# Optimization experiments

Hardware: AMD Instinct MI355X
Metric: run time of the kernel (lower is better)

Reference implementation:

```python
import jax, jax.numpy as jnp
import numpy as np

N = 8192        # n_nodes
NFEAT = 512
NHID = 256
AVG_DEG = 32
K = 64          # mean_kwargs k
TEMP = 1.0      # mean_kwargs temperature


def setup_inputs() -> dict:
    key = jax.random.key(0)
    ks = jax.random.split(key, 5)
    x = jax.random.normal(ks[0], (N, NFEAT), jnp.float32)
    edge_index = jax.random.randint(ks[1], (2, N * AVG_DEG), 0, N, dtype=jnp.int64)
    W1 = jax.random.normal(ks[2], (NFEAT, NHID), jnp.float32) / np.sqrt(NFEAT)
    b1 = jnp.zeros((NHID,), jnp.float32)
    W2 = jax.random.normal(ks[3], (NHID, NHID), jnp.float32) / np.sqrt(NHID)
    b2 = jnp.zeros((NHID,), jnp.float32)
    return {"x": x, "edge_index": edge_index, "W1": W1, "b1": b1, "W2": W2, "b2": b2}


def _gcn_norm(edge_index, n, dtype):
    # PyG gcn_norm: add self-loops (weight 1), deg over col, sym normalization
    loops = jnp.arange(n, dtype=edge_index.dtype)
    row = jnp.concatenate([edge_index[0], loops])
    col = jnp.concatenate([edge_index[1], loops])
    w = jnp.ones(row.shape[0], dtype)
    deg = jnp.zeros((n,), dtype).at[col].add(w)
    dis = jnp.where(deg > 0, jax.lax.rsqrt(jnp.where(deg > 0, deg, 1.0)), 0.0)
    return row, col, dis[row] * w * dis[col]


def _soft_k_medoid(row, col, w, x):
    # soft_weighted_medoid_k_neighborhood(A, x, k=K, temperature=TEMP, with_weight_correction=True)
    n, d = x.shape
    A = jnp.zeros((n, n), x.dtype).at[row, col].add(w)   # coalesced dense adjacency
    topk_a, topk_idx = jax.lax.top_k(A, K)               # [n, K] neighbor weights / ids
    xk = x[topk_idx]                                     # [n, K, d]
    sq = jnp.sum(xk * xk, axis=-1)                       # [n, K]
    G = jnp.einsum('nkd,nld->nkl', xk, xk)               # Gram per node
    d2 = jnp.maximum(sq[:, :, None] + sq[:, None, :] - 2.0 * G, 0.0)
    pos = d2 > 0
    dist = jnp.where(pos, jnp.sqrt(jnp.where(pos, d2, 1.0)), 0.0)  # safe sqrt (grad-safe)
    # weighted sum of distances to each top-k candidate j: c[n,j] = sum_l a[n,l] * ||x_l - x_j||
    c = jnp.einsum('nl,nlj->nj', topk_a, dist)
    c = jnp.where(topk_a == 0, jnp.finfo(x.dtype).max, c)
    soft = jax.nn.softmax(-c / TEMP, axis=-1)            # [n, K]
    soft = soft * topk_a                                 # with_weight_correction
    soft = soft / jnp.sum(soft, axis=-1, keepdims=True)
    row_sum = jnp.sum(A, axis=-1)                        # preserve neighborhood mass
    return row_sum[:, None] * jnp.einsum('nk,nkd->nd', soft, xk)


def reference(x, edge_index, W1, b1, W2, b2):
    n = x.shape[0]
    row, col, w = _gcn_norm(edge_index, n, x.dtype)
    h = jax.nn.relu(_soft_k_medoid(row, col, w, x @ W1) + b1)   # gc1 + relu (dropout: eval = identity)
    return jax.nn.relu(_soft_k_medoid(row, col, w, h @ W2) + b2)  # gc2 + relu
```

## Files before the change

kernel.cpp:

```cpp
#include <hip/hip_runtime.h>

typedef _Float16 half2v __attribute__((ext_vector_type(2)));
typedef _Float16 half4 __attribute__((ext_vector_type(4)));
typedef _Float16 half8 __attribute__((ext_vector_type(8)));
typedef float f32x4 __attribute__((ext_vector_type(4)));

#define NNODE 8192
#define NHID  256
#define RCAP  128
#define KCAP  64

__global__ void k_init(int* deg, int* rowcnt, int* flag, const void* edges) {
    int i = blockIdx.x * blockDim.x + threadIdx.x;
    if (i < NNODE) { deg[i] = 0; rowcnt[i] = 0; }
    if (i == 0) {
        const long long* e = (const long long*)edges;
        int ok = 1;
        for (int k = 0; k < 64; ++k) { long long v = e[k]; if (v < 0 || v >= NNODE) ok = 0; }
        *flag = ok;
    }
}

__global__ void k_build(const void* edges, const int* flag, int* rowcnt, int* nbr,
                        int* deg, int E) {
    int i = blockIdx.x * blockDim.x + threadIdx.x;
    int total = E + NNODE;
    if (i >= total) return;
    int r, c;
    if (i < E) {
        if (*flag) {
            const long long* e = (const long long*)edges;
            r = (int)e[i]; c = (int)e[E + i];
        } else {
            const int* e = (const int*)edges;
            r = e[i]; c = e[E + i];
        }
    } else { r = i - E; c = r; }
    int pos = atomicAdd(&rowcnt[r], 1);
    if (pos < RCAP) nbr[r * RCAP + pos] = c;
    atomicAdd(&deg[c], 1);
}

__global__ __launch_bounds__(128) void k_dedup(const int* __restrict__ nbr,
                                               const int* __restrict__ rowcnt,
                                               const int* __restrict__ deg,
                                               int* __restrict__ cols,
                                               float* __restrict__ wout,
                                               float* __restrict__ rsum) {
    __shared__ int lc[RCAP];
    __shared__ float lw[RCAP];
    __shared__ unsigned char kp[RCAP];
    __shared__ int s_cw[2];
    __shared__ float s_rw[2];
    const int r = blockIdx.x, t = threadIdx.x;
    const int wid = t >> 6, lane = t & 63;
    int n = rowcnt[r]; if (n > RCAP) n = RCAP;
    if (t < n) lc[t] = nbr[r * RCAP + t];
    __syncthreads();
    float dr = 1.f / sqrtf((float)deg[r]);
    bool keep = false; float wv = 0.f;
    if (t < n) {
        int c = lc[t];
        int mult = 0; bool first = true;
        for (int i = 0; i < n; ++i) {
            int ci = lc[i];
            if (ci == c) { mult++; if (i < t) first = false; }
        }
        keep = first;
        if (first) wv = (float)mult * dr * (1.f / sqrtf((float)deg[c]));
    }
    kp[t] = keep ? 1 : 0; lw[t] = wv;
    float rv = wv;
#pragma unroll
    for (int d = 1; d < 64; d <<= 1) rv += __shfl_xor(rv, d, 64);
    unsigned long long b = __ballot(keep);
    int pre = __popcll(b & ((1ull << lane) - 1ull));
    int cw = __popcll(b);
    if (lane == 0) { s_cw[wid] = cw; s_rw[wid] = rv; }
    __syncthreads();
    int total = s_cw[0] + s_cw[1];
    if (t == 0) rsum[r] = s_rw[0] + s_rw[1];
    const int base = r * KCAP;
    if (total <= KCAP) {
        int off = (wid ? s_cw[0] : 0) + pre;
        if (keep) { cols[base + off] = lc[t]; wout[base + off] = wv; }
        for (int m = total + t; m < KCAP; m += 128) { cols[base + m] = r; wout[base + m] = 0.f; }
    } else if (t == 0) {
        for (int s = 0; s < KCAP; ++s) {
            int best = -1;
            for (int i = 0; i < n; ++i) {
                if (!kp[i]) continue;
                if (best < 0 || lw[i] > lw[best] ||
                    (lw[i] == lw[best] && lc[i] < lc[best])) best = i;
            }
            cols[base + s] = lc[best]; wout[base + s] = lw[best]; kp[best] = 0;
        }
    }
}

__global__ void k_splitT(const float* __restrict__ W, _Float16* __restrict__ hiT, int Kdim) {
    int idx = blockIdx.x * 256 + threadIdx.x;
    if (idx >= Kdim * NHID) return;
    int k = idx >> 8, n = idx & 255;
    hiT[(size_t)n * Kdim + k] = (_Float16)W[idx];
}

#define GLS 72

__global__ __launch_bounds__(256) void k_gemm(
    const float* __restrict__ Af32, const _Float16* __restrict__ Ahi,
    const _Float16* __restrict__ BT, _Float16* __restrict__ Chi, int K, int af32) {
    __shared__ _Float16 sA[64][GLS];
    __shared__ _Float16 sB[64][GLS];
    const int t = threadIdx.x;
    const int bm = blockIdx.x * 64, bn = blockIdx.y * 64;
    const int lane = t & 63, L15 = lane & 15, q = lane >> 4;
    const int w = t >> 6, wr = w >> 1, wc = w & 1;
    f32x4 acc[2][2];
#pragma unroll
    for (int a = 0; a < 2; ++a)
#pragma unroll
        for (int b = 0; b < 2; ++b) acc[a][b] = (f32x4){0.f, 0.f, 0.f, 0.f};

    for (int k0 = 0; k0 < K; k0 += 64) {
        if (af32) {
#pragma unroll
            for (int i = 0; i < 4; ++i) {
                int row = i * 16 + (t >> 4), kc = (t & 15) * 4;
                float4 v = *(const float4*)(Af32 + (size_t)(bm + row) * K + k0 + kc);
                half4 h;
                h[0] = (_Float16)v.x; h[1] = (_Float16)v.y;
                h[2] = (_Float16)v.z; h[3] = (_Float16)v.w;
                *(half4*)&sA[row][kc] = h;
            }
        } else {
#pragma unroll
            for (int i = 0; i < 2; ++i) {
                int row = i * 32 + (t >> 3), ch = t & 7;
                *(half8*)&sA[row][ch * 8] =
                    *(const half8*)(Ahi + (size_t)(bm + row) * K + k0 + ch * 8);
            }
        }
#pragma unroll
        for (int i = 0; i < 2; ++i) {
            int row = i * 32 + (t >> 3), ch = t & 7;
            *(half8*)&sB[row][ch * 8] =
                *(const half8*)(BT + (size_t)(bn + row) * K + k0 + ch * 8);
        }
        __syncthreads();
#pragma unroll
        for (int ks = 0; ks < 2; ++ks) {
            const int ko = ks * 32 + q * 8;
            half8 ah[2], bh[2];
#pragma unroll
            for (int tr = 0; tr < 2; ++tr)
                ah[tr] = *(const half8*)&sA[32 * wr + 16 * tr + L15][ko];
#pragma unroll
            for (int tc = 0; tc < 2; ++tc)
                bh[tc] = *(const half8*)&sB[32 * wc + 16 * tc + L15][ko];
#pragma unroll
            for (int tr = 0; tr < 2; ++tr)
#pragma unroll
                for (int tc = 0; tc < 2; ++tc)
                    acc[tr][tc] = __builtin_amdgcn_mfma_f32_16x16x32_f16(ah[tr], bh[tc], acc[tr][tc], 0, 0, 0);
        }
        __syncthreads();
    }
#pragma unroll
    for (int tr = 0; tr < 2; ++tr)
#pragma unroll
        for (int tc = 0; tc < 2; ++tc)
#pragma unroll
            for (int r = 0; r < 4; ++r) {
                int rowg = bm + 32 * wr + 16 * tr + q * 4 + r;
                int colg = bn + 32 * wc + 16 * tc + L15;
                Chi[(size_t)rowg * NHID + colg] = (_Float16)acc[tr][tc][r];
            }
}

#define MS 264

__global__ __launch_bounds__(256, 4) void k_medoid(
    const _Float16* __restrict__ Xhi,
    const float* __restrict__ bias,
    float* __restrict__ OutF, _Float16* __restrict__ OutHi,
    const int* __restrict__ cols, const float* __restrict__ wts,
    const float* __restrict__ rsum, int writeH) {
    __shared__ _Float16 sh[64][MS];
    __shared__ float s_a[64];
    __shared__ float s_sq[64];
    __shared__ float s_cpart[2][64];
    __shared__ float s_u[64];
    __shared__ int   s_cols[64];
    __shared__ float s_red[4][288];

    const int node = blockIdx.x;
    const int t = threadIdx.x;
    const int w = t >> 6, lane = t & 63;
    const int L15 = lane & 15, q = lane >> 4;
    const int wr = w >> 1, wc = w & 1;

    if (t < 64) { s_cols[t] = cols[node * KCAP + t]; s_a[t] = wts[node * KCAP + t]; }
    __syncthreads();

    {
        const int ch = t & 31, rr = t >> 5;
#pragma unroll
        for (int i = 0; i < 8; ++i) {
            int l = i * 8 + rr;
            *(half8*)&sh[l][ch * 8] = *(const half8*)(Xhi + ((size_t)s_cols[l] << 8) + ch * 8);
        }
    }
    __syncthreads();

    f32x4 acc[2][2];
#pragma unroll
    for (int a = 0; a < 2; ++a)
#pragma unroll
        for (int b = 0; b < 2; ++b) acc[a][b] = (f32x4){0.f, 0.f, 0.f, 0.f};
#pragma unroll
    for (int ks = 0; ks < 8; ++ks) {
        const int ko = ks * 32 + q * 8;
        half8 ah[2], bh[2];
#pragma unroll
        for (int tr = 0; tr < 2; ++tr) ah[tr] = *(const half8*)&sh[32 * wr + 16 * tr + L15][ko];
#pragma unroll
        for (int tc = 0; tc < 2; ++tc) bh[tc] = *(const half8*)&sh[32 * wc + 16 * tc + L15][ko];
#pragma unroll
        for (int tr = 0; tr < 2; ++tr)
#pragma unroll
            for (int tc = 0; tc < 2; ++tc)
                acc[tr][tc] = __builtin_amdgcn_mfma_f32_16x16x32_f16(ah[tr], bh[tc], acc[tr][tc], 0, 0, 0);
    }

#pragma unroll
    for (int tr = 0; tr < 2; ++tr)
#pragma unroll
        for (int tc = 0; tc < 2; ++tc)
            if (32 * wr + 16 * tr == 32 * wc + 16 * tc) {
#pragma unroll
                for (int r = 0; r < 4; ++r)
                    if (L15 == q * 4 + r) s_sq[32 * wr + 16 * tr + L15] = acc[tr][tc][r];
            }
    __syncthreads();

#pragma unroll
    for (int tc = 0; tc < 2; ++tc) {
        const int colg = 32 * wc + 16 * tc + L15;
        const float sqc = s_sq[colg];
        float pj = 0.f;
#pragma unroll
        for (int tr = 0; tr < 2; ++tr)
#pragma unroll
            for (int r = 0; r < 4; ++r) {
                int rowg = 32 * wr + 16 * tr + q * 4 + r;
                float d2 = s_sq[rowg] + sqc - 2.f * acc[tr][tc][r];
                float dist = d2 > 0.f ? __builtin_amdgcn_sqrtf(d2) : 0.f;
                pj = fmaf(s_a[rowg], dist, pj);
            }
        pj += __shfl_xor(pj, 16, 64);
        pj += __shfl_xor(pj, 32, 64);
        if (q == 0) s_cpart[wr][colg] = pj;
    }
    __syncthreads();

    if (w == 0) {
        int j = lane;
        float c = s_cpart[0][j] + s_cpart[1][j];
        float aj = s_a[j];
        bool valid = aj > 0.f;
        float cv = valid ? c : 3.4e38f;
        float mn = cv;
#pragma unroll
        for (int d = 1; d < 64; d <<= 1) mn = fminf(mn, __shfl_xor(mn, d, 64));
        float e = valid ? __expf(mn - c) * aj : 0.f;
        float s = e;
#pragma unroll
        for (int d = 1; d < 64; d <<= 1) s += __shfl_xor(s, d, 64);
        s_u[j] = e * (rsum[node] / s);
    }
    __syncthreads();

    const int oct = t & 31, jb = t >> 5;
    float accd[8] = {0.f, 0.f, 0.f, 0.f, 0.f, 0.f, 0.f, 0.f};
#pragma unroll
    for (int jj = 0; jj < 8; ++jj) {
        int j = jb * 8 + jj;
        float u = s_u[j];
        half8 xv = *(const half8*)&sh[j][8 * oct];
#pragma unroll
        for (int e = 0; e < 8; ++e) accd[e] = fmaf(u, (float)xv[e], accd[e]);
    }
#pragma unroll
    for (int e = 0; e < 8; ++e) accd[e] += __shfl_xor(accd[e], 32, 64);
    if (lane < 32) {
#pragma unroll
        for (int e = 0; e < 8; ++e) s_red[w][9 * oct + e] = accd[e];
    }
    __syncthreads();
    const int idx = 9 * (t >> 3) + (t & 7);
    float o = s_red[0][idx] + s_red[1][idx] + s_red[2][idx] + s_red[3][idx];
    float res = fmaxf(o + bias[t], 0.f);
    size_t oi = (size_t)node * NHID + t;
    if (writeH) OutHi[oi] = (_Float16)res;
    else        OutF[oi] = res;
}

extern "C" void kernel_launch(void* const* d_in, const int* in_sizes, int n_in,
                              void* d_out, int out_size, void* d_ws, size_t ws_size,
                              hipStream_t stream) {
    const float* x  = (const float*)d_in[0];
    const void*  ei = d_in[1];
    const float* W1 = (const float*)d_in[2];
    const float* b1 = (const float*)d_in[3];
    const float* W2 = (const float*)d_in[4];
    const float* b2 = (const float*)d_in[5];
    float* out = (float*)d_out;
    const int E = in_sizes[1] / 2;

    char* p = (char*)d_ws;
    auto alloc = [&](size_t bytes) { char* q = p; p += (bytes + 255) & ~(size_t)255; return q; };
    int*      deg    = (int*)alloc((size_t)NNODE * 4);
    int*      rowcnt = (int*)alloc((size_t)NNODE * 4);
    int*      flag   = (int*)alloc(256);
    int*      colsA  = (int*)alloc((size_t)NNODE * KCAP * 4);
    float*    wA     = (float*)alloc((size_t)NNODE * KCAP * 4);
    float*    rsum   = (float*)alloc((size_t)NNODE * 4);
    _Float16* w1T    = (_Float16*)alloc((size_t)512 * NHID * 2);
    _Float16* w2T    = (_Float16*)alloc((size_t)NHID * NHID * 2);
    _Float16* X1hi   = (_Float16*)alloc((size_t)NNODE * NHID * 2);
    _Float16* Hhi    = (_Float16*)alloc((size_t)NNODE * NHID * 2);
    int* nbr = (int*)alloc((size_t)NNODE * RCAP * 4);

    k_init<<<(NNODE + 255) / 256, 256, 0, stream>>>(deg, rowcnt, flag, ei);
    k_build<<<(E + NNODE + 255) / 256, 256, 0, stream>>>(ei, flag, rowcnt, nbr, deg, E);
    k_dedup<<<NNODE, 128, 0, stream>>>(nbr, rowcnt, deg, colsA, wA, rsum);

    k_splitT<<<(512 * NHID + 255) / 256, 256, 0, stream>>>(W1, w1T, 512);
    k_splitT<<<(NHID * NHID + 255) / 256, 256, 0, stream>>>(W2, w2T, 256);

    k_gemm<<<dim3(NNODE / 64, NHID / 64), 256, 0, stream>>>(x, nullptr, w1T, X1hi, 512, 1);
    k_medoid<<<NNODE, 256, 0, stream>>>(X1hi, b1, nullptr, Hhi, colsA, wA, rsum, 1);
    k_gemm<<<dim3(NNODE / 64, NHID / 64), 256, 0, stream>>>(nullptr, Hhi, w2T, X1hi, 256, 0);
    k_medoid<<<NNODE, 256, 0, stream>>>(X1hi, b2, out, nullptr, colsA, wA, rsum, 0);
}
```

Before: 218.4 us.

## Fuse graph build with first GEMM, dedup into medoid, and halve medoid LDS

Merges the edge scatter with the first GEMM into one launch by block range, and folds the per-row dedup into the first medoid kernel. The weight transposes are dropped: the GEMMs read fp32 W directly and transpose while staging into shared memory. The medoid kernel now stages neighbour features in two 128-column halves, which cuts LDS so more blocks fit per CU (launch bounds 6), and reads the first half back from global memory for the final weighted sum. The aim is fewer launches, fewer intermediate round-trips and higher occupancy. The costs are extra global re-reads and strided, bank-conflicting shared-memory writes in the W transpose.

Result: no change. 220.7 us (+1.1%).

```diff
diff --git a/kernel.cpp b/kernel.cpp
--- a/kernel.cpp
+++ b/kernel.cpp
@@ -1,6 +1,5 @@
 #include <hip/hip_runtime.h>
 
-typedef _Float16 half2v __attribute__((ext_vector_type(2)));
 typedef _Float16 half4 __attribute__((ext_vector_type(4)));
 typedef _Float16 half8 __attribute__((ext_vector_type(8)));
 typedef float f32x4 __attribute__((ext_vector_type(4)));
@@ -9,118 +8,35 @@
 #define NHID  256
 #define RCAP  128
 #define KCAP  64
-
-__global__ void k_init(int* deg, int* rowcnt, int* flag, const void* edges) {
-    int i = blockIdx.x * blockDim.x + threadIdx.x;
-    if (i < NNODE) { deg[i] = 0; rowcnt[i] = 0; }
-    if (i == 0) {
-        const long long* e = (const long long*)edges;
-        int ok = 1;
-        for (int k = 0; k < 64; ++k) { long long v = e[k]; if (v < 0 || v >= NNODE) ok = 0; }
-        *flag = ok;
-    }
-}
-
-__global__ void k_build(const void* edges, const int* flag, int* rowcnt, int* nbr,
-                        int* deg, int E) {
-    int i = blockIdx.x * blockDim.x + threadIdx.x;
-    int total = E + NNODE;
-    if (i >= total) return;
-    int r, c;
-    if (i < E) {
-        if (*flag) {
-            const long long* e = (const long long*)edges;
-            r = (int)e[i]; c = (int)e[E + i];
-        } else {
-            const int* e = (const int*)edges;
-            r = e[i]; c = e[E + i];
-        }
-    } else { r = i - E; c = r; }
-    int pos = atomicAdd(&rowcnt[r], 1);
-    if (pos < RCAP) nbr[r * RCAP + pos] = c;
-    atomicAdd(&deg[c], 1);
-}
-
-__global__ __launch_bounds__(128) void k_dedup(const int* __restrict__ nbr,
-                                               const int* __restrict__ rowcnt,
-                                               const int* __restrict__ deg,
-                                               int* __restrict__ cols,
-                                               float* __restrict__ wout,
-                                               float* __restrict__ rsum) {
-    __shared__ int lc[RCAP];
-    __shared__ float lw[RCAP];
-    __shared__ unsigned char kp[RCAP];
-    __shared__ int s_cw[2];
-    __shared__ float s_rw[2];
-    const int r = blockIdx.x, t = threadIdx.x;
-    const int wid = t >> 6, lane = t & 63;
-    int n = rowcnt[r]; if (n > RCAP) n = RCAP;
-    if (t < n) lc[t] = nbr[r * RCAP + t];
-    __syncthreads();
-    float dr = 1.f / sqrtf((float)deg[r]);
-    bool keep = false; float wv = 0.f;
-    if (t < n) {
-        int c = lc[t];
-        int mult = 0; bool first = true;
-        for (int i = 0; i < n; ++i) {
-            int ci = lc[i];
-            if (ci == c) { mult++; if (i < t) first = false; }
-        }
-        keep = first;
-        if (first) wv = (float)mult * dr * (1.f / sqrtf((float)deg[c]));
-    }
-    kp[t] = keep ? 1 : 0; lw[t] = wv;
-    float rv = wv;
-#pragma unroll
-    for (int d = 1; d < 64; d <<= 1) rv += __shfl_xor(rv, d, 64);
-    unsigned long long b = __ballot(keep);
-    int pre = __popcll(b & ((1ull << lane) - 1ull));
-    int cw = __popcll(b);
-    if (lane == 0) { s_cw[wid] = cw; s_rw[wid] = rv; }
-    __syncthreads();
-    int total = s_cw[0] + s_cw[1];
-    if (t == 0) rsum[r] = s_rw[0] + s_rw[1];
-    const int base = r * KCAP;
-    if (total <= KCAP) {
-        int off = (wid ? s_cw[0] : 0) + pre;
-        if (keep) { cols[base + off] = lc[t]; wout[base + off] = wv; }
-        for (int m = total + t; m < KCAP; m += 128) { cols[base + m] = r; wout[base + m] = 0.f; }
-    } else if (t == 0) {
-        for (int s = 0; s < KCAP; ++s) {
-            int best = -1;
-            for (int i = 0; i < n; ++i) {
-                if (!kp[i]) continue;
-                if (best < 0 || lw[i] > lw[best] ||
-                    (lw[i] == lw[best] && lc[i] < lc[best])) best = i;
-            }
-            cols[base + s] = lc[best]; wout[base + s] = lw[best]; kp[best] = 0;
-        }
-    }
-}
-
-__global__ void k_splitT(const float* __restrict__ W, _Float16* __restrict__ hiT, int Kdim) {
-    int idx = blockIdx.x * 256 + threadIdx.x;
-    if (idx >= Kdim * NHID) return;
-    int k = idx >> 8, n = idx & 255;
-    hiT[(size_t)n * Kdim + k] = (_Float16)W[idx];
-}
-
-#define GLS 72
-
-__global__ __launch_bounds__(256) void k_gemm(
-    const float* __restrict__ Af32, const _Float16* __restrict__ Ahi,
-    const _Float16* __restrict__ BT, _Float16* __restrict__ Chi, int K, int af32) {
-    __shared__ _Float16 sA[64][GLS];
-    __shared__ _Float16 sB[64][GLS];
+#define GLS   72
+#define SK    136
+
+struct SmemGemm { _Float16 sA[64][GLS]; _Float16 sB[64][GLS]; };
+
+struct DedupScratch {
+    int lc[RCAP]; float lw[RCAP]; unsigned char kp[RCAP];
+    int cw[2]; float rw[2];
+};
+
+struct SmemMedoid {
+    union { _Float16 sh[64][SK]; DedupScratch dd; } u;
+    float s_a[64]; float s_sq[64]; float s_cpart[2][64]; float s_u[64];
+    int s_cols[64]; float s_red[4][288]; float s_rsum;
+};
+
+__device__ __forceinline__ void gemm_body(
+    char* smraw, const float* __restrict__ Af32, const _Float16* __restrict__ Ahi,
+    const float* __restrict__ W, _Float16* __restrict__ Chi,
+    int K, int af32, int bm, int bn) {
+    SmemGemm& sm = *(SmemGemm*)smraw;
     const int t = threadIdx.x;
-    const int bm = blockIdx.x * 64, bn = blockIdx.y * 64;
     const int lane = t & 63, L15 = lane & 15, q = lane >> 4;
     const int w = t >> 6, wr = w >> 1, wc = w & 1;
     f32x4 acc[2][2];
 #pragma unroll
     for (int a = 0; a < 2; ++a)
 #pragma unroll
-        for (int b = 0; b < 2; ++b) acc[a][b] = (f32x4){0.f, 0.f, 0.f, 0.f};
+        for (int b2 = 0; b2 < 2; ++b2) acc[a][b2] = (f32x4){0.f, 0.f, 0.f, 0.f};
 
     for (int k0 = 0; k0 < K; k0 += 64) {
         if (af32) {
@@ -131,21 +47,24 @@
                 half4 h;
                 h[0] = (_Float16)v.x; h[1] = (_Float16)v.y;
                 h[2] = (_Float16)v.z; h[3] = (_Float16)v.w;
-                *(half4*)&sA[row][kc] = h;
+                *(half4*)&sm.sA[row][kc] = h;
             }
         } else {
 #pragma unroll
             for (int i = 0; i < 2; ++i) {
                 int row = i * 32 + (t >> 3), ch = t & 7;
-                *(half8*)&sA[row][ch * 8] =
+                *(half8*)&sm.sA[row][ch * 8] =
                     *(const half8*)(Ahi + (size_t)(bm + row) * K + k0 + ch * 8);
             }
         }
 #pragma unroll
-        for (int i = 0; i < 2; ++i) {
-            int row = i * 32 + (t >> 3), ch = t & 7;
-            *(half8*)&sB[row][ch * 8] =
-                *(const half8*)(BT + (size_t)(bn + row) * K + k0 + ch * 8);
+        for (int i = 0; i < 4; ++i) {
+            int krow = i * 16 + (t >> 4), nc4 = (t & 15) * 4;
+            float4 v = *(const float4*)(W + (size_t)(k0 + krow) * NHID + bn + nc4);
+            sm.sB[nc4 + 0][krow] = (_Float16)v.x;
+            sm.sB[nc4 + 1][krow] = (_Float16)v.y;
+            sm.sB[nc4 + 2][krow] = (_Float16)v.z;
+            sm.sB[nc4 + 3][krow] = (_Float16)v.w;
         }
         __syncthreads();
 #pragma unroll
@@ -154,10 +73,10 @@
             half8 ah[2], bh[2];
 #pragma unroll
             for (int tr = 0; tr < 2; ++tr)
-                ah[tr] = *(const half8*)&sA[32 * wr + 16 * tr + L15][ko];
+                ah[tr] = *(const half8*)&sm.sA[32 * wr + 16 * tr + L15][ko];
 #pragma unroll
             for (int tc = 0; tc < 2; ++tc)
-                bh[tc] = *(const half8*)&sB[32 * wc + 16 * tc + L15][ko];
+                bh[tc] = *(const half8*)&sm.sB[32 * wc + 16 * tc + L15][ko];
 #pragma unroll
             for (int tr = 0; tr < 2; ++tr)
 #pragma unroll
@@ -178,59 +97,44 @@
             }
 }
 
-#define MS 264
-
-__global__ __launch_bounds__(256, 4) void k_medoid(
-    const _Float16* __restrict__ Xhi,
-    const float* __restrict__ bias,
-    float* __restrict__ OutF, _Float16* __restrict__ OutHi,
-    const int* __restrict__ cols, const float* __restrict__ wts,
-    const float* __restrict__ rsum, int writeH) {
-    __shared__ _Float16 sh[64][MS];
-    __shared__ float s_a[64];
-    __shared__ float s_sq[64];
-    __shared__ float s_cpart[2][64];
-    __shared__ float s_u[64];
-    __shared__ int   s_cols[64];
-    __shared__ float s_red[4][288];
-
-    const int node = blockIdx.x;
+__device__ __forceinline__ void medoid_core(
+    SmemMedoid& sm, const _Float16* __restrict__ Xhi, const float* __restrict__ bias,
+    float* __restrict__ OutF, _Float16* __restrict__ OutHi, int node, int writeH) {
     const int t = threadIdx.x;
     const int w = t >> 6, lane = t & 63;
     const int L15 = lane & 15, q = lane >> 4;
     const int wr = w >> 1, wc = w & 1;
 
-    if (t < 64) { s_cols[t] = cols[node * KCAP + t]; s_a[t] = wts[node * KCAP + t]; }
-    __syncthreads();
-
-    {
-        const int ch = t & 31, rr = t >> 5;
-#pragma unroll
-        for (int i = 0; i < 8; ++i) {
-            int l = i * 8 + rr;
-            *(half8*)&sh[l][ch * 8] = *(const half8*)(Xhi + ((size_t)s_cols[l] << 8) + ch * 8);
-        }
-    }
-    __syncthreads();
-
     f32x4 acc[2][2];
 #pragma unroll
     for (int a = 0; a < 2; ++a)
 #pragma unroll
         for (int b = 0; b < 2; ++b) acc[a][b] = (f32x4){0.f, 0.f, 0.f, 0.f};
-#pragma unroll
-    for (int ks = 0; ks < 8; ++ks) {
-        const int ko = ks * 32 + q * 8;
-        half8 ah[2], bh[2];
-#pragma unroll
-        for (int tr = 0; tr < 2; ++tr) ah[tr] = *(const half8*)&sh[32 * wr + 16 * tr + L15][ko];
-#pragma unroll
-        for (int tc = 0; tc < 2; ++tc) bh[tc] = *(const half8*)&sh[32 * wc + 16 * tc + L15][ko];
-#pragma unroll
-        for (int tr = 0; tr < 2; ++tr)
-#pragma unroll
-            for (int tc = 0; tc < 2; ++tc)
-                acc[tr][tc] = __builtin_amdgcn_mfma_f32_16x16x32_f16(ah[tr], bh[tc], acc[tr][tc], 0, 0, 0);
+
+    const int ch = t & 15, rr = t >> 4;
+    for (int phase = 0; phase < 2; ++phase) {
+#pragma unroll
+        for (int i = 0; i < 4; ++i) {
+            int l = i * 16 + rr;
+            *(half8*)&sm.u.sh[l][ch * 8] =
+                *(const half8*)(Xhi + ((size_t)sm.s_cols[l] << 8) + phase * 128 + ch * 8);
+        }
+        __syncthreads();
+#pragma unroll
+        for (int ks = 0; ks < 4; ++ks) {
+            const int ko = ks * 32 + q * 8;
+            half8 ah[2], bh[2];
+#pragma unroll
+            for (int tr = 0; tr < 2; ++tr) ah[tr] = *(const half8*)&sm.u.sh[32 * wr + 16 * tr + L15][ko];
+#pragma unroll
+            for (int tc = 0; tc < 2; ++tc) bh[tc] = *(const half8*)&sm.u.sh[32 * wc + 16 * tc + L15][ko];
+#pragma unroll
+            for (int tr = 0; tr < 2; ++tr)
+#pragma unroll
+                for (int tc = 0; tc < 2; ++tc)
+                    acc[tr][tc] = __builtin_amdgcn_mfma_f32_16x16x32_f16(ah[tr], bh[tc], acc[tr][tc], 0, 0, 0);
+        }
+        if (phase == 0) __syncthreads();
     }
 
 #pragma unroll
@@ -240,34 +144,39 @@
             if (32 * wr + 16 * tr == 32 * wc + 16 * tc) {
 #pragma unroll
                 for (int r = 0; r < 4; ++r)
-                    if (L15 == q * 4 + r) s_sq[32 * wr + 16 * tr + L15] = acc[tr][tc][r];
-            }
-    __syncthreads();
-
+                    if (L15 == q * 4 + r) sm.s_sq[32 * wr + 16 * tr + L15] = acc[tr][tc][r];
+            }
+    __syncthreads();
+
+    f32x4 sq4[2], a4[2];
+#pragma unroll
+    for (int tr = 0; tr < 2; ++tr) {
+        sq4[tr] = *(const f32x4*)&sm.s_sq[32 * wr + 16 * tr + 4 * q];
+        a4[tr]  = *(const f32x4*)&sm.s_a [32 * wr + 16 * tr + 4 * q];
+    }
 #pragma unroll
     for (int tc = 0; tc < 2; ++tc) {
         const int colg = 32 * wc + 16 * tc + L15;
-        const float sqc = s_sq[colg];
+        const float sqc = sm.s_sq[colg];
         float pj = 0.f;
 #pragma unroll
         for (int tr = 0; tr < 2; ++tr)
 #pragma unroll
             for (int r = 0; r < 4; ++r) {
-                int rowg = 32 * wr + 16 * tr + q * 4 + r;
-                float d2 = s_sq[rowg] + sqc - 2.f * acc[tr][tc][r];
+                float d2 = sq4[tr][r] + sqc - 2.f * acc[tr][tc][r];
                 float dist = d2 > 0.f ? __builtin_amdgcn_sqrtf(d2) : 0.f;
-                pj = fmaf(s_a[rowg], dist, pj);
+                pj = fmaf(a4[tr][r], dist, pj);
             }
         pj += __shfl_xor(pj, 16, 64);
         pj += __shfl_xor(pj, 32, 64);
-        if (q == 0) s_cpart[wr][colg] = pj;
+        if (q == 0) sm.s_cpart[wr][colg] = pj;
     }
     __syncthreads();
 
     if (w == 0) {
         int j = lane;
-        float c = s_cpart[0][j] + s_cpart[1][j];
-        float aj = s_a[j];
+        float c = sm.s_cpart[0][j] + sm.s_cpart[1][j];
+        float aj = sm.s_a[j];
         bool valid = aj > 0.f;
         float cv = valid ? c : 3.4e38f;
         float mn = cv;
@@ -277,7 +186,7 @@
         float s = e;
 #pragma unroll
         for (int d = 1; d < 64; d <<= 1) s += __shfl_xor(s, d, 64);
-        s_u[j] = e * (rsum[node] / s);
+        sm.s_u[j] = e * (sm.s_rsum / s);
     }
     __syncthreads();
 
@@ -286,8 +195,10 @@
 #pragma unroll
     for (int jj = 0; jj < 8; ++jj) {
         int j = jb * 8 + jj;
-        float u = s_u[j];
-        half8 xv = *(const half8*)&sh[j][8 * oct];
+        float u = sm.s_u[j];
+        half8 xv;
+        if (oct < 16) xv = *(const half8*)(Xhi + ((size_t)sm.s_cols[j] << 8) + oct * 8);
+        else          xv = *(const half8*)&sm.u.sh[j][(oct - 16) * 8];
 #pragma unroll
         for (int e = 0; e < 8; ++e) accd[e] = fmaf(u, (float)xv[e], accd[e]);
     }
@@ -295,15 +206,140 @@
     for (int e = 0; e < 8; ++e) accd[e] += __shfl_xor(accd[e], 32, 64);
     if (lane < 32) {
 #pragma unroll
-        for (int e = 0; e < 8; ++e) s_red[w][9 * oct + e] = accd[e];
+        for (int e = 0; e < 8; ++e) sm.s_red[w][9 * oct + e] = accd[e];
     }
     __syncthreads();
     const int idx = 9 * (t >> 3) + (t & 7);
-    float o = s_red[0][idx] + s_red[1][idx] + s_red[2][idx] + s_red[3][idx];
+    float o = sm.s_red[0][idx] + sm.s_red[1][idx] + sm.s_red[2][idx] + sm.s_red[3][idx];
     float res = fmaxf(o + bias[t], 0.f);
     size_t oi = (size_t)node * NHID + t;
     if (writeH) OutHi[oi] = (_Float16)res;
     else        OutF[oi] = res;
+}
+
+__global__ __launch_bounds__(256) void k_s1(
+    const float* __restrict__ x, const float* __restrict__ W1, const void* edges,
+    int* rowcnt, int* nbr, int* deg, int E, _Float16* __restrict__ X1) {
+    if ((int)blockIdx.x < 512) {
+        __shared__ __align__(16) char smem[sizeof(SmemGemm)];
+        int g = blockIdx.x;
+        gemm_body(smem, x, nullptr, W1, X1, 512, 1, (g >> 2) * 64, (g & 3) * 64);
+    } else {
+        __shared__ int sflag;
+        const int t = threadIdx.x;
+        if (t < 64) {
+            const long long* e = (const long long*)edges;
+            long long v = e[t];
+            unsigned long long bad = __ballot(v < 0 || v >= (long long)NNODE);
+            if (t == 0) sflag = (bad == 0) ? 1 : 0;
+        }
+        __syncthreads();
+        const int fl = sflag;
+        int i = ((int)blockIdx.x - 512) * 256 + t;
+        if (i >= E + NNODE) return;
+        int r, c;
+        if (i < E) {
+            if (fl) {
+                const long long* e = (const long long*)edges;
+                r = (int)e[i]; c = (int)e[E + i];
+            } else {
+                const int* e = (const int*)edges;
+                r = e[i]; c = e[E + i];
+            }
+        } else { r = i - E; c = r; }
+        int pos = atomicAdd(&rowcnt[r], 1);
+        if (pos < RCAP) nbr[r * RCAP + pos] = c;
+        atomicAdd(&deg[c], 1);
+    }
+}
+
+__global__ __launch_bounds__(256, 6) void k_medoid1(
+    const _Float16* __restrict__ X, const float* __restrict__ b1,
+    _Float16* __restrict__ Hh,
+    const int* __restrict__ nbr, const int* __restrict__ rowcnt,
+    const int* __restrict__ deg,
+    int* __restrict__ cols, float* __restrict__ wA, float* __restrict__ rsum) {
+    __shared__ __align__(16) SmemMedoid sm;
+    const int r = blockIdx.x, t = threadIdx.x;
+    const int w = t >> 6, lane = t & 63;
+
+    int n = rowcnt[r]; if (n > RCAP) n = RCAP;
+    if (t < n) sm.u.dd.lc[t] = nbr[r * RCAP + t];
+    __syncthreads();
+    float dr = 1.f / sqrtf((float)deg[r]);
+    bool keep = false; float wv = 0.f; int myc = 0;
+    if (t < n) {
+        myc = sm.u.dd.lc[t];
+        int mult = 0; bool first = true;
+        for (int i = 0; i < n; ++i) {
+            int ci = sm.u.dd.lc[i];
+            if (ci == myc) { mult++; if (i < t) first = false; }
+        }
+        keep = first;
+        if (first) wv = (float)mult * dr * (1.f / sqrtf((float)deg[myc]));
+    }
+    if (t < RCAP) { sm.u.dd.kp[t] = keep ? 1 : 0; sm.u.dd.lw[t] = wv; }
+    int pre = 0;
+    if (w < 2) {
+        float rv = wv;
+#pragma unroll
+        for (int d = 1; d < 64; d <<= 1) rv += __shfl_xor(rv, d, 64);
+        unsigned long long b = __ballot(keep);
+        pre = __popcll(b & ((1ull << lane) - 1ull));
+        int cw = __popcll(b);
+        if (lane == 0) { sm.u.dd.cw[w] = cw; sm.u.dd.rw[w] = rv; }
+    }
+    __syncthreads();
+    int total = sm.u.dd.cw[0] + sm.u.dd.cw[1];
+    float rs = sm.u.dd.rw[0] + sm.u.dd.rw[1];
+    if (t == 0) { rsum[r] = rs; sm.s_rsum = rs; }
+    const int base = r * KCAP;
+    if (total <= KCAP) {
+        if (w < 2 && keep) {
+            int off = (w ? sm.u.dd.cw[0] : 0) + pre;
+            cols[base + off] = myc; wA[base + off] = wv;
+            sm.s_cols[off] = myc;   sm.s_a[off] = wv;
+        }
+        for (int m = total + t; m < KCAP; m += 256) {
+            cols[base + m] = r; wA[base + m] = 0.f;
+            sm.s_cols[m] = r;   sm.s_a[m] = 0.f;
+        }
+    } else if (t == 0) {
+        for (int s = 0; s < KCAP; ++s) {
+            int best = -1;
+            for (int i = 0; i < n; ++i) {
+                if (!sm.u.dd.kp[i]) continue;
+                if (best < 0 || sm.u.dd.lw[i] > sm.u.dd.lw[best] ||
+                    (sm.u.dd.lw[i] == sm.u.dd.lw[best] && sm.u.dd.lc[i] < sm.u.dd.lc[best])) best = i;
+            }
+            cols[base + s] = sm.u.dd.lc[best]; wA[base + s] = sm.u.dd.lw[best];
+            sm.s_cols[s] = sm.u.dd.lc[best];   sm.s_a[s] = sm.u.dd.lw[best];
+            sm.u.dd.kp[best] = 0;
+        }
+    }
+    __syncthreads();
+
+    medoid_core(sm, X, b1, nullptr, Hh, r, 1);
+}
+
+__global__ __launch_bounds__(256) void k_gemm2(
+    const _Float16* __restrict__ Hh, const float* __restrict__ W2,
+    _Float16* __restrict__ X2) {
+    __shared__ __align__(16) char smem[sizeof(SmemGemm)];
+    gemm_body(smem, nullptr, Hh, W2, X2, 256, 0, blockIdx.x * 64, blockIdx.y * 64);
+}
+
+__global__ __launch_bounds__(256, 6) void k_medoid2(
+    const _Float16* __restrict__ X, const float* __restrict__ b2,
+    float* __restrict__ out,
+    const int* __restrict__ cols, const float* __restrict__ wts,
+    const float* __restrict__ rsum) {
+    __shared__ __align__(16) SmemMedoid sm;
+    const int node = blockIdx.x, t = threadIdx.x;
+    if (t < 64) { sm.s_cols[t] = cols[node * KCAP + t]; sm.s_a[t] = wts[node * KCAP + t]; }
+    if (t == 0) sm.s_rsum = rsum[node];
+    __syncthreads();
+    medoid_core(sm, X, b2, out, nullptr, node, 0);
 }
 
 extern "C" void kernel_launch(void* const* d_in, const int* in_sizes, int n_in,
@@ -320,27 +356,21 @@
 
     char* p = (char*)d_ws;
     auto alloc = [&](size_t bytes) { char* q = p; p += (bytes + 255) & ~(size_t)255; return q; };
-    int*      deg    = (int*)alloc((size_t)NNODE * 4);
-    int*      rowcnt = (int*)alloc((size_t)NNODE * 4);
-    int*      flag   = (int*)alloc(256);
+    int*      cnt   = (int*)alloc((size_t)2 * NNODE * 4);
+    int*      deg    = cnt;
+    int*      rowcnt = cnt + NNODE;
     int*      colsA  = (int*)alloc((size_t)NNODE * KCAP * 4);
-    float*    wA     = (float*)alloc((size_t)NNODE * KCAP * 4);
+    float*    wAr    = (float*)alloc((size_t)NNODE * KCAP * 4);
     float*    rsum   = (float*)alloc((size_t)NNODE * 4);
-    _Float16* w1T    = (_Float16*)alloc((size_t)512 * NHID * 2);
-    _Float16* w2T    = (_Float16*)alloc((size_t)NHID * NHID * 2);
-    _Float16* X1hi   = (_Float16*)alloc((size_t)NNODE * NHID * 2);
-    _Float16* Hhi    = (_Float16*)alloc((size_t)NNODE * NHID * 2);
-    int* nbr = (int*)alloc((size_t)NNODE * RCAP * 4);
-
-    k_init<<<(NNODE + 255) / 256, 256, 0, stream>>>(deg, rowcnt, flag, ei);
-    k_build<<<(E + NNODE + 255) / 256, 256, 0, stream>>>(ei, flag, rowcnt, nbr, deg, E);
-    k_dedup<<<NNODE, 128, 0, stream>>>(nbr, rowcnt, deg, colsA, wA, rsum);
-
-    k_splitT<<<(512 * NHID + 255) / 256, 256, 0, stream>>>(W1, w1T, 512);
-    k_splitT<<<(NHID * NHID + 255) / 256, 256, 0, stream>>>(W2, w2T, 256);
-
-    k_gemm<<<dim3(NNODE / 64, NHID / 64), 256, 0, stream>>>(x, nullptr, w1T, X1hi, 512, 1);
-    k_medoid<<<NNODE, 256, 0, stream>>>(X1hi, b1, nullptr, Hhi, colsA, wA, rsum, 1);
-    k_gemm<<<dim3(NNODE / 64, NHID / 64), 256, 0, stream>>>(nullptr, Hhi, w2T, X1hi, 256, 0);
-    k_medoid<<<NNODE, 256, 0, stream>>>(X1hi, b2, out, nullptr, colsA, wA, rsum, 0);
-}
+    _Float16* X1     = (_Float16*)alloc((size_t)NNODE * NHID * 2);
+    _Float16* Hh     = (_Float16*)alloc((size_t)NNODE * NHID * 2);
+    int*      nbr    = (int*)alloc((size_t)NNODE * RCAP * 4);
+
+    const int nscat = (E + NNODE + 255) / 256;
+
+    hipMemsetAsync(cnt, 0, (size_t)2 * NNODE * 4, stream);
+    k_s1<<<512 + nscat, 256, 0, stream>>>(x, W1, ei, rowcnt, nbr, deg, E, X1);
+    k_medoid1<<<NNODE, 256, 0, stream>>>(X1, b1, Hh, nbr, rowcnt, deg, colsA, wAr, rsum);
+    k_gemm2<<<dim3(NNODE / 64, NHID / 64), 256, 0, stream>>>(Hh, W2, X1);
+    k_medoid2<<<NNODE, 256, 0, stream>>>(X1, b2, out, colsA, wAr, rsum);
+}
```
